# Kernel optimization log

Hardware: AMD Instinct MI355X
Metric: run time of the kernel (lower is better)

The kernel has to match this reference:

```python
import jax, jax.numpy as jnp
import numpy as np

N_NODES = 100000
N_EDGES = 1600000
EMB = 128
HID = 128
N_CLASSES = 10
N_GRAPHS = 512
EPS = 1e-5


def sage_conv(x, src, dst, Wl, Wr, b):
    # PyG SAGEConv: out = lin_l(mean_{j in N(i)} x_j) + lin_r(x_i)
    msg = x[src]  # [E, d] gather
    agg = jax.ops.segment_sum(msg, dst, num_segments=N_NODES)
    deg = jax.ops.segment_sum(jnp.ones((src.shape[0],), x.dtype), dst, num_segments=N_NODES)
    agg = agg / jnp.maximum(deg, 1.0)[:, None]
    return agg @ Wl + x @ Wr + b


def setup_inputs() -> dict:
    key = jax.random.key(0)
    ks = jax.random.split(key, 20)
    x = jax.random.normal(ks[0], (N_NODES, EMB), dtype=jnp.float32)
    edge_index = jax.random.randint(ks[1], (2, N_EDGES), 0, N_NODES, dtype=jnp.int64)
    batch = jnp.sort(jax.random.randint(ks[2], (N_NODES,), 0, N_GRAPHS, dtype=jnp.int64))
    s = lambda k, shp, fan: jax.random.normal(k, shp, dtype=jnp.float32) * (1.0 / np.sqrt(fan))
    inp = {
        'x': x, 'edge_index': edge_index, 'batch': batch,
        'bn_gamma': jnp.ones((EMB,), jnp.float32),
        'bn_beta': jnp.zeros((EMB,), jnp.float32),
        'bn_mean': jax.random.normal(ks[3], (EMB,), jnp.float32) * 0.1,
        'bn_var': jax.random.uniform(ks[4], (EMB,), jnp.float32, 0.5, 1.5),
        'Wl1': s(ks[5], (EMB, HID), EMB), 'Wr1': s(ks[6], (EMB, HID), EMB), 'b1': jnp.zeros((HID,), jnp.float32),
        'Wl2': s(ks[7], (HID, HID), HID), 'Wr2': s(ks[8], (HID, HID), HID), 'b2': jnp.zeros((HID,), jnp.float32),
        'Wl3': s(ks[9], (HID, HID), HID), 'Wr3': s(ks[10], (HID, HID), HID), 'b3': jnp.zeros((HID,), jnp.float32),
        'Wm1': s(ks[11], (HID, HID), HID), 'bm1': jnp.zeros((HID,), jnp.float32),
        'Wm2': s(ks[12], (HID, N_CLASSES), HID), 'bm2': jnp.zeros((N_CLASSES,), jnp.float32),
    }
    return inp


def reference(x, edge_index, batch, bn_gamma, bn_beta, bn_mean, bn_var,
              Wl1, Wr1, b1, Wl2, Wr2, b2, Wl3, Wr3, b3, Wm1, bm1, Wm2, bm2):
    src, dst = edge_index[0], edge_index[1]
    # BatchNorm (eval mode, running stats); dropout is identity in eval
    h = (x - bn_mean) * jax.lax.rsqrt(bn_var + EPS) * bn_gamma + bn_beta
    h = jax.nn.relu(sage_conv(h, src, dst, Wl1, Wr1, b1))
    h = jax.nn.relu(sage_conv(h, src, dst, Wl2, Wr2, b2))
    h = jax.nn.relu(sage_conv(h, src, dst, Wl3, Wr3, b3))
    # global mean pool over graphs
    summed = jax.ops.segment_sum(h, batch, num_segments=N_GRAPHS)
    counts = jax.ops.segment_sum(jnp.ones((h.shape[0],), h.dtype), batch, num_segments=N_GRAPHS)
    g = summed / jnp.maximum(counts, 1.0)[:, None]
    g = g @ Wm1 + bm1
    g = g @ Wm2 + bm2
    return jax.nn.log_softmax(g, axis=1)
```

## Files before the change

kernel.cpp:

```cpp
#include <hip/hip_runtime.h>

#define NN 100000
#define NE 1600000
#define CH 128
#define NG 512
#define NC 10
#define NBK 782
#define NBA 800
#define EPB 2000
#define WB  384
#define BB  12500
#define GB  391
#define BPB 64

typedef float floatx4 __attribute__((ext_vector_type(4)));
typedef float floatx2 __attribute__((ext_vector_type(2)));
union f8frag { uint2 u; long long l; };

__device__ __forceinline__ float b2f(unsigned short u) {
    return __uint_as_float(((unsigned)u) << 16);
}
__device__ __forceinline__ unsigned short f2b(float f) {
    unsigned u = __float_as_uint(f);
    u += 0x7FFFu + ((u >> 16) & 1u);
    return (unsigned short)(u >> 16);
}
__device__ __forceinline__ float wlo(unsigned w) { return __uint_as_float(w << 16); }
__device__ __forceinline__ float whi(unsigned w) { return __uint_as_float(w & 0xFFFF0000u); }

__device__ __forceinline__ float ldf(const void* p, long i, int isb) {
    return isb ? b2f(((const unsigned short*)p)[i]) : ((const float*)p)[i];
}
__device__ __forceinline__ int ldi(const void* p, long i, int is64) {
    const int* q = (const int*)p;
    return is64 ? q[2 * i] : q[i];
}
__device__ __forceinline__ unsigned pk4_fp8(float f0, float f1, float f2, float f3) {
    int u = 0;
    u = __builtin_amdgcn_cvt_pk_fp8_f32(f0, f1, u, false);
    u = __builtin_amdgcn_cvt_pk_fp8_f32(f2, f3, u, true);
    return (unsigned)u;
}
__device__ __forceinline__ unsigned char f2f8(float v) {
    return (unsigned char)(__builtin_amdgcn_cvt_pk_fp8_f32(v, v, 0, false) & 0xFF);
}
__device__ __forceinline__ int detect_isb(const void* gamma) {
    return (*(const unsigned*)gamma == 0x3F800000u) ? 0 : 1;
}
__device__ __forceinline__ int detect_is64(const void* eidx) {
    const unsigned* e = (const unsigned*)eidx;
    return ((e[1] | e[3] | e[5] | e[7]) == 0u) ? 1 : 0;
}

__global__ __launch_bounds__(256) void prep_k(const void* __restrict__ x, const void* __restrict__ gamma,
                     const void* __restrict__ beta, const void* __restrict__ mean,
                     const void* __restrict__ var, const void* __restrict__ eidx,
                     const void* __restrict__ batch,
                     const void* W1, const void* W2, const void* W3,
                     const void* W4, const void* W5, const void* W6,
                     unsigned char* __restrict__ WT8,
                     unsigned* __restrict__ f80,
                     int* __restrict__ gcnt,
                     int* __restrict__ gse) {
    __shared__ int hist[NBK];
    int isb = detect_isb(gamma);
    if (blockIdx.x < WB) {
        int idx = blockIdx.x * 256 + threadIdx.x;
        int w = idx >> 14;
        int k = (idx >> 7) & 127;
        int n = idx & 127;
        const void* W = (w == 0) ? W1 : (w == 1) ? W2 : (w == 2) ? W3
                      : (w == 3) ? W4 : (w == 4) ? W5 : W6;
        float v = ldf(W, (long)k * CH + n, isb);
        WT8[(w << 14) + n * CH + k] = f2f8(v);
        return;
    }
    if (blockIdx.x >= WB + BB + NBA) {
        int i = (blockIdx.x - (WB + BB + NBA)) * 256 + threadIdx.x;
        if (i >= NN) return;
        int is64 = detect_is64(eidx);
        int b1v = ldi(batch, i, is64);
        int b0v = (i == 0) ? -1 : ldi(batch, (long)i - 1, is64);
        for (int g = b0v + 1; g <= b1v; ++g) gse[g] = i;
        if (i == NN - 1)
            for (int g = b1v + 1; g <= NG; ++g) gse[g] = NN;
        return;
    }
    if (blockIdx.x >= WB + BB) {
        int pb = blockIdx.x - (WB + BB);
        int is64 = detect_is64(eidx);
        int t = threadIdx.x;
        for (int b = t; b < NBK; b += 256) hist[b] = 0;
        __syncthreads();
        long e0 = (long)pb * EPB;
        for (int i = t; i < EPB; i += 256) {
            int d = ldi(eidx, (long)NE + e0 + i, is64);
            atomicAdd(&hist[d >> 7], 1);
        }
        __syncthreads();
        for (int b = t; b < NBK; b += 256) gcnt[(long)pb * NBK + b] = hist[b];
        return;
    }
    long i4 = ((long)(blockIdx.x - WB) * 256 + threadIdx.x) * 4;
    if (i4 >= (long)NN * CH) return;
    int c = (int)(i4 & (CH - 1));
    float xv[4], g[4], b[4], m[4], v[4];
    if (isb) {
        uint2 U = *(const uint2*)((const unsigned short*)x + i4);
        xv[0] = wlo(U.x); xv[1] = whi(U.x); xv[2] = wlo(U.y); xv[3] = whi(U.y);
        uint2 G = *(const uint2*)((const unsigned short*)gamma + c);
        g[0] = wlo(G.x); g[1] = whi(G.x); g[2] = wlo(G.y); g[3] = whi(G.y);
        uint2 B = *(const uint2*)((const unsigned short*)beta + c);
        b[0] = wlo(B.x); b[1] = whi(B.x); b[2] = wlo(B.y); b[3] = whi(B.y);
        uint2 M = *(const uint2*)((const unsigned short*)mean + c);
        m[0] = wlo(M.x); m[1] = whi(M.x); m[2] = wlo(M.y); m[3] = whi(M.y);
        uint2 V = *(const uint2*)((const unsigned short*)var + c);
        v[0] = wlo(V.x); v[1] = whi(V.x); v[2] = wlo(V.y); v[3] = whi(V.y);
    } else {
        float4 X = *(const float4*)((const float*)x + i4);
        xv[0] = X.x; xv[1] = X.y; xv[2] = X.z; xv[3] = X.w;
        float4 G = *(const float4*)((const float*)gamma + c);
        g[0] = G.x; g[1] = G.y; g[2] = G.z; g[3] = G.w;
        float4 B = *(const float4*)((const float*)beta + c);
        b[0] = B.x; b[1] = B.y; b[2] = B.z; b[3] = B.w;
        float4 M = *(const float4*)((const float*)mean + c);
        m[0] = M.x; m[1] = M.y; m[2] = M.z; m[3] = M.w;
        float4 V = *(const float4*)((const float*)var + c);
        v[0] = V.x; v[1] = V.y; v[2] = V.z; v[3] = V.w;
    }
    float o[4];
#pragma unroll
    for (int j = 0; j < 4; ++j)
        o[j] = (xv[j] - m[j]) * rsqrtf(v[j] + 1e-5f) * g[j] + b[j];
    f80[i4 >> 2] = pk4_fp8(o[0], o[1], o[2], o[3]);
}

__global__ __launch_bounds__(64) void colscan_k(const int* __restrict__ gcnt,
                                                int* __restrict__ colscan,
                                                int* __restrict__ btot) {
    int b = blockIdx.x;
    int lane = threadIdx.x;
    int carry = 0;
    for (int base = 0; base < NBA; base += 64) {
        int blk = base + lane;
        int v = (blk < NBA) ? gcnt[(long)blk * NBK + b] : 0;
        int x = v;
        for (int off = 1; off < 64; off <<= 1) {
            int y = __shfl_up(x, off);
            if (lane >= off) x += y;
        }
        if (blk < NBA) colscan[(long)b * NBA + blk] = carry + x - v;
        carry += __shfl(x, 63);
    }
    if (lane == 0) btot[b] = carry;
}

__global__ __launch_bounds__(1024) void bscan_k(const int* __restrict__ btot,
                                                int* __restrict__ bbase) {
    __shared__ int s[1024];
    int t = threadIdx.x;
    int v = (t < NBK) ? btot[t] : 0;
    s[t] = v;
    __syncthreads();
    for (int off = 1; off < 1024; off <<= 1) {
        int add = (t >= off) ? s[t - off] : 0;
        __syncthreads();
        s[t] += add;
        __syncthreads();
    }
    if (t < NBK) bbase[t] = s[t] - v;
}

__global__ __launch_bounds__(256) void partC_k(const void* __restrict__ eidx,
                                               const int* __restrict__ colscan,
                                               const int* __restrict__ bbase,
                                               unsigned* __restrict__ epair) {
    __shared__ int pos[NBK];
    int is64 = detect_is64(eidx);
    int t = threadIdx.x;
    int pb = (int)(blockIdx.x & 7) * (NBA / 8) + (int)(blockIdx.x >> 3);
    for (int b = t; b < NBK; b += 256)
        pos[b] = bbase[b] + colscan[(long)b * NBA + pb];
    __syncthreads();
    long e0 = (long)pb * EPB;
    for (int i = t; i < EPB; i += 256) {
        int sv = ldi(eidx, e0 + i, is64);
        int d  = ldi(eidx, (long)NE + e0 + i, is64);
        int b = d >> 7;
        int p = atomicAdd(&pos[b], 1);
        epair[p] = ((unsigned)(d & 127) << 20) | (unsigned)sv;
    }
}

__global__ __launch_bounds__(256) void csrfill_k(const unsigned* __restrict__ epair,
                                                 const int* __restrict__ bbase,
                                                 const int* __restrict__ btot,
                                                 int* __restrict__ row_ptr,
                                                 int* __restrict__ esrc) {
    __shared__ int hist[128];
    __shared__ int s[128];
    __shared__ int wcur[128];
    int bkt = blockIdx.x;
    int t = threadIdx.x;
    if (t < 128) hist[t] = 0;
    __syncthreads();
    int e0 = bbase[bkt], n = btot[bkt];
    for (int i = t; i < n; i += 256) atomicAdd(&hist[epair[e0 + i] >> 20], 1);
    __syncthreads();
    int v = (t < 128) ? hist[t] : 0;
    if (t < 128) s[t] = v;
    for (int off = 1; off < 128; off <<= 1) {
        __syncthreads();
        int add = (t < 128 && t >= off) ? s[t - off] : 0;
        __syncthreads();
        if (t < 128) s[t] += add;
    }
    __syncthreads();
    if (t < 128) {
        int excl = s[t] - v;
        int node = (bkt << 7) + t;
        int base = e0 + excl;
        wcur[t] = base;
        if (node < NN) row_ptr[node] = base;
        if (node == 0) row_ptr[NN] = NE;
    }
    __syncthreads();
    for (int i = t; i < n; i += 256) {
        unsigned pv = epair[e0 + i];
        int q = atomicAdd(&wcur[pv >> 20], 1);
        esrc[q] = (int)(pv & 0xFFFFFu);
    }
}

__device__ __forceinline__ uint4 gld1(const uint4* __restrict__ f8in4,
                                      const int* __restrict__ esrc,
                                      int ee, int s1v, int h) {
    bool val = ee < s1v;
    int ec = max(min(ee, s1v - 1), 0);
    int idx = esrc[ec];
    idx = val ? idx : 0;
    uint4 u = f8in4[(size_t)idx * 8 + h];
    if (!val) { u.x = 0u; u.y = 0u; u.z = 0u; u.w = 0u; }
    return u;
}

#define ACC8(u) do { \
    a0 += __builtin_amdgcn_cvt_pk_f32_fp8((int)(u).x, false); \
    a1 += __builtin_amdgcn_cvt_pk_f32_fp8((int)(u).x, true);  \
    a2 += __builtin_amdgcn_cvt_pk_f32_fp8((int)(u).y, false); \
    a3 += __builtin_amdgcn_cvt_pk_f32_fp8((int)(u).y, true);  \
    a4 += __builtin_amdgcn_cvt_pk_f32_fp8((int)(u).z, false); \
    a5 += __builtin_amdgcn_cvt_pk_f32_fp8((int)(u).z, true);  \
    a6 += __builtin_amdgcn_cvt_pk_f32_fp8((int)(u).w, false); \
    a7 += __builtin_amdgcn_cvt_pk_f32_fp8((int)(u).w, true);  \
} while (0)

__global__ __launch_bounds__(1024, 8) void flayer_k(const uint4* __restrict__ f8in4,
                                                const int* __restrict__ row_ptr,
                                                const int* __restrict__ esrc,
                                                const uint4* __restrict__ Wl4,
                                                const uint4* __restrict__ Wr4,
                                                const void* __restrict__ bias,
                                                const void* __restrict__ gamma,
                                                unsigned char* __restrict__ out8) {
    __shared__ unsigned char WlS[16384];
    __shared__ unsigned char WrS[16384];
    __shared__ unsigned char Ag[BPB][144];
    __shared__ unsigned char Sf[BPB][144];
    const int tid = threadIdx.x;
    const int wv = tid >> 6;
    const int lane = tid & 63;
    const int sub = lane >> 4;
    const int l15 = lane & 15;
    const int row0 = blockIdx.x * BPB;

    {
        int wrow = tid >> 3, h16 = (tid & 7) * 16;
        int dst = wrow * 128 + (h16 ^ ((wrow & 7) << 4));
        *(uint4*)&WlS[dst] = Wl4[tid];
        *(uint4*)&WrS[dst] = Wr4[tid];
    }
    if (tid < BPB * 8) {
        int r = tid >> 3, h = tid & 7;
        int rs = min(row0 + r, NN - 1);
        *(uint4*)&Sf[r][h * 16] = f8in4[(size_t)rs * 8 + h];
    }

    const int nl = wv * 4 + sub;
    const int node = row0 + nl;
    const int nc = min(node, NN - 1);
    const int s0 = row_ptr[nc];
    const int s1v = (node < NN) ? row_ptr[nc + 1] : s0;
    const int par = l15 >> 3;
    const int h = l15 & 7;
    floatx2 a0 = {0.f, 0.f}, a1 = {0.f, 0.f}, a2 = {0.f, 0.f}, a3 = {0.f, 0.f};
    floatx2 a4 = {0.f, 0.f}, a5 = {0.f, 0.f}, a6 = {0.f, 0.f}, a7 = {0.f, 0.f};
    uint4 q0, q1, q2, q3;
    int ee = s0 + par;
    q0 = gld1(f8in4, esrc, ee,     s1v, h);
    q1 = gld1(f8in4, esrc, ee + 2, s1v, h);
    q2 = gld1(f8in4, esrc, ee + 4, s1v, h);
    q3 = gld1(f8in4, esrc, ee + 6, s1v, h);
    ee += 8;
    for (;;) {
        if (!__any(ee < s1v)) break;
        ACC8(q0); q0 = gld1(f8in4, esrc, ee, s1v, h); ee += 2;
        if (!__any(ee < s1v)) break;
        ACC8(q1); q1 = gld1(f8in4, esrc, ee, s1v, h); ee += 2;
        if (!__any(ee < s1v)) break;
        ACC8(q2); q2 = gld1(f8in4, esrc, ee, s1v, h); ee += 2;
        if (!__any(ee < s1v)) break;
        ACC8(q3); q3 = gld1(f8in4, esrc, ee, s1v, h); ee += 2;
    }
    ACC8(q0); ACC8(q1); ACC8(q2); ACC8(q3);
#define CMB(x) do { x[0] += __shfl_xor(x[0], 8); x[1] += __shfl_xor(x[1], 8); } while (0)
    CMB(a0); CMB(a1); CMB(a2); CMB(a3); CMB(a4); CMB(a5); CMB(a6); CMB(a7);
#undef CMB
    if (par == 0) {
        float inv = 1.0f / (float)max(s1v - s0, 1);
        uint4 o;
        o.x = pk4_fp8(a0[0] * inv, a0[1] * inv, a1[0] * inv, a1[1] * inv);
        o.y = pk4_fp8(a2[0] * inv, a2[1] * inv, a3[0] * inv, a3[1] * inv);
        o.z = pk4_fp8(a4[0] * inv, a4[1] * inv, a5[0] * inv, a5[1] * inv);
        o.w = pk4_fp8(a6[0] * inv, a6[1] * inv, a7[0] * inv, a7[1] * inv);
        *(uint4*)&Ag[nl][h * 16] = o;
    }
    __syncthreads();

    const int rt0 = (wv >> 2) * 16;
    const int n0 = (wv & 3) * 32;
    const int quad = sub;
    floatx4 acc[2];
    acc[0] = (floatx4)0.f; acc[1] = (floatx4)0.f;
#pragma unroll
    for (int chunk = 0; chunk < 8; ++chunk) {
        const unsigned char* WS = (chunk < 4) ? WlS : WrS;
        const int k8 = ((chunk & 3) * 4 + quad) * 8;
        const int r0 = n0 + l15;
        const int r1 = n0 + 16 + l15;
        f8frag b0, b1, a;
        b0.u = *(const uint2*)&WS[r0 * 128 + (k8 ^ ((r0 & 7) << 4))];
        b1.u = *(const uint2*)&WS[r1 * 128 + (k8 ^ ((r1 & 7) << 4))];
        if (chunk < 4) a.u = *(const uint2*)&Ag[rt0 + l15][k8];
        else           a.u = *(const uint2*)&Sf[rt0 + l15][k8];
        acc[0] = __builtin_amdgcn_mfma_f32_16x16x32_fp8_fp8(a.l, b0.l, acc[0], 0, 0, 0);
        acc[1] = __builtin_amdgcn_mfma_f32_16x16x32_fp8_fp8(a.l, b1.l, acc[1], 0, 0, 0);
    }
    const int isb = detect_isb(gamma);
    float bv0 = ldf(bias, n0 + l15, isb);
    float bv1 = ldf(bias, n0 + 16 + l15, isb);
    __syncthreads();
#pragma unroll
    for (int tc = 0; tc < 2; ++tc) {
        int col = n0 + tc * 16 + l15;
        float bv = tc ? bv1 : bv0;
#pragma unroll
        for (int r = 0; r < 4; ++r) {
            int row = rt0 + quad * 4 + r;
            Ag[row][col] = f2f8(fmaxf(acc[tc][r] + bv, 0.f));
        }
    }
    __syncthreads();
    if (tid < BPB * 8) {
        int r = tid >> 3, h2 = tid & 7;
        if (row0 + r < NN)
            *(uint4*)(out8 + (size_t)(row0 + r) * CH + h2 * 16) = *(const uint4*)&Ag[r][h2 * 16];
    }
}

__global__ __launch_bounds__(512) void poolmlp_k(const uint2* __restrict__ f8h,
                                                 const int* __restrict__ gse,
                                                 const void* __restrict__ gamma,
                                                 const void* __restrict__ Wm1, const void* __restrict__ bm1,
                                                 const void* __restrict__ Wm2, const void* __restrict__ bm2,
                                                 void* __restrict__ dout) {
    int g = blockIdx.x;
    int t = threadIdx.x;
    int wv = t >> 6;
    int lane = t & 63;
    int sub = lane >> 4;
    int l15 = lane & 15;
    int isb = detect_isb(gamma);
    __shared__ float red[8][128];
    __shared__ float pl[CH];
    __shared__ float hv[CH];
    __shared__ float logit[NC];
    __shared__ float lse;
    int s0 = gse[g], s1 = gse[g + 1];
    floatx2 a0 = {0.f, 0.f}, a1 = {0.f, 0.f}, a2 = {0.f, 0.f}, a3 = {0.f, 0.f};
    for (int n = s0 + wv * 4 + sub; n < s1; n += 32) {
        uint2 u = f8h[n * 16 + l15];
        a0 += __builtin_amdgcn_cvt_pk_f32_fp8((int)u.x, false);
        a1 += __builtin_amdgcn_cvt_pk_f32_fp8((int)u.x, true);
        a2 += __builtin_amdgcn_cvt_pk_f32_fp8((int)u.y, false);
        a3 += __builtin_amdgcn_cvt_pk_f32_fp8((int)u.y, true);
    }
#pragma unroll
    for (int sh = 16; sh <= 32; sh <<= 1) {
        a0[0] += __shfl_xor(a0[0], sh); a0[1] += __shfl_xor(a0[1], sh);
        a1[0] += __shfl_xor(a1[0], sh); a1[1] += __shfl_xor(a1[1], sh);
        a2[0] += __shfl_xor(a2[0], sh); a2[1] += __shfl_xor(a2[1], sh);
        a3[0] += __shfl_xor(a3[0], sh); a3[1] += __shfl_xor(a3[1], sh);
    }
    if (sub == 0) {
        int c = l15 * 8;
        red[wv][c + 0] = a0[0]; red[wv][c + 1] = a0[1];
        red[wv][c + 2] = a1[0]; red[wv][c + 3] = a1[1];
        red[wv][c + 4] = a2[0]; red[wv][c + 5] = a2[1];
        red[wv][c + 6] = a3[0]; red[wv][c + 7] = a3[1];
    }
    __syncthreads();
    if (t < CH) {
        float s = 0.f;
#pragma unroll
        for (int w = 0; w < 8; ++w) s += red[w][t];
        pl[t] = s / (float)max(s1 - s0, 1);
    }
    __syncthreads();
    if (t < CH) {
        float acc = ldf(bm1, t, isb);
        for (int k = 0; k < CH; ++k) acc += pl[k] * ldf(Wm1, (long)k * CH + t, isb);
        hv[t] = acc;
    }
    __syncthreads();
    if (t < NC) {
        float a2v = ldf(bm2, t, isb);
        for (int k = 0; k < CH; ++k) a2v += hv[k] * ldf(Wm2, (long)k * NC + t, isb);
        logit[t] = a2v;
    }
    __syncthreads();
    if (t == 0) {
        float m = -1e30f;
        for (int i = 0; i < NC; ++i) m = fmaxf(m, logit[i]);
        float s = 0.f;
        for (int i = 0; i < NC; ++i) s += expf(logit[i] - m);
        lse = m + logf(s);
    }
    __syncthreads();
    if (t < NC) {
        float o = logit[t] - lse;
        if (isb) ((unsigned short*)dout)[g * NC + t] = f2b(o);
        else     ((float*)dout)[g * NC + t] = o;
    }
}

extern "C" void kernel_launch(void* const* d_in, const int* in_sizes, int n_in,
                              void* d_out, int out_size, void* d_ws, size_t ws_size,
                              hipStream_t stream) {
    const void* x     = d_in[0];
    const void* eidx  = d_in[1];
    const void* batch = d_in[2];
    const void* gamma = d_in[3];
    const void* beta  = d_in[4];
    const void* mean  = d_in[5];
    const void* var   = d_in[6];
    const void* Wl1 = d_in[7],  *Wr1 = d_in[8],  *b1 = d_in[9];
    const void* Wl2 = d_in[10], *Wr2 = d_in[11], *b2 = d_in[12];
    const void* Wl3 = d_in[13], *Wr3 = d_in[14], *b3 = d_in[15];
    const void* Wm1 = d_in[16], *bm1 = d_in[17], *Wm2 = d_in[18], *bm2 = d_in[19];

    char* ws = (char*)d_ws;
    size_t off = 0;
    auto alloc = [&](size_t bytes) -> void* {
        void* p = (void*)(ws + off);
        off = (off + bytes + 255) & ~(size_t)255;
        return p;
    };
    int*   row_ptr = (int*)alloc((size_t)(NN + 1) * 4);
    int*   esrc    = (int*)alloc((size_t)NE * 4);
    unsigned* epair = (unsigned*)alloc((size_t)NE * 4);
    int*   btot    = (int*)alloc((size_t)NBK * 4);
    int*   bbase   = (int*)alloc((size_t)NBK * 4);
    int*   gse     = (int*)alloc((size_t)(NG + 1) * 4);
    unsigned char* WT8 = (unsigned char*)alloc((size_t)6 * CH * CH);
    unsigned char* f8A = (unsigned char*)alloc((size_t)NN * CH);
    unsigned char* f8B = (unsigned char*)alloc((size_t)NN * CH);
    (void)ws_size; (void)in_sizes; (void)n_in; (void)out_size;

    int* gcnt    = (int*)f8B;
    int* colscan = (int*)(f8B + (((size_t)NBA * NBK * 4 + 255) & ~(size_t)255));

    prep_k<<<WB + BB + NBA + GB, 256, 0, stream>>>(x, gamma, beta, mean, var, eidx, batch,
                                                   Wl1, Wr1, Wl2, Wr2, Wl3, Wr3,
                                                   WT8, (unsigned*)f8A, gcnt, gse);
    colscan_k<<<NBK, 64, 0, stream>>>(gcnt, colscan, btot);
    bscan_k<<<1, 1024, 0, stream>>>(btot, bbase);
    partC_k<<<NBA, 256, 0, stream>>>(eidx, colscan, bbase, epair);
    csrfill_k<<<NBK, 256, 0, stream>>>(epair, bbase, btot, row_ptr, esrc);

    const uint4* W4l1 = (const uint4*)(WT8 + 0 * CH * CH);
    const uint4* W4r1 = (const uint4*)(WT8 + 1 * CH * CH);
    const uint4* W4l2 = (const uint4*)(WT8 + 2 * CH * CH);
    const uint4* W4r2 = (const uint4*)(WT8 + 3 * CH * CH);
    const uint4* W4l3 = (const uint4*)(WT8 + 4 * CH * CH);
    const uint4* W4r3 = (const uint4*)(WT8 + 5 * CH * CH);

    const int fl_grid = (NN + BPB - 1) / BPB;

    flayer_k<<<fl_grid, 1024, 0, stream>>>((const uint4*)f8A, row_ptr, esrc,
                                           W4l1, W4r1, b1, gamma, f8B);
    flayer_k<<<fl_grid, 1024, 0, stream>>>((const uint4*)f8B, row_ptr, esrc,
                                           W4l2, W4r2, b2, gamma, f8A);
    flayer_k<<<fl_grid, 1024, 0, stream>>>((const uint4*)f8A, row_ptr, esrc,
                                           W4l3, W4r3, b3, gamma, f8B);

    poolmlp_k<<<NG, 512, 0, stream>>>((const uint2*)f8B, gse, gamma,
                                      Wm1, bm1, Wm2, bm2, d_out);
}
```

Before: 359.2 us.

## Split fused SAGE layer into plane-major gather and GEMM kernels

Stores fp8 node features in four 32-channel planes instead of row-major 128-byte rows. Each fused layer kernel becomes a gather kernel, which averages one plane per block over neighbors, and a separate GEMM kernel that reads the aggregated buffer. Gathering one plane at a time shrinks the working set of random neighbor reads so it may stay in cache. The cost is an extra kernel launch per layer and a write plus re-read of the aggregate buffer, which reuses the edge-pair scratch memory.

```diff
diff --git a/kernel.cpp b/kernel.cpp
--- a/kernel.cpp
+++ b/kernel.cpp
@@ -12,6 +12,7 @@
 #define BB  12500
 #define GB  391
 #define BPB 64
+#define PLN ((size_t)NN * 4)
 
 typedef float floatx4 __attribute__((ext_vector_type(4)));
 typedef float floatx2 __attribute__((ext_vector_type(2)));
@@ -132,7 +133,9 @@
 #pragma unroll
     for (int j = 0; j < 4; ++j)
         o[j] = (xv[j] - m[j]) * rsqrtf(v[j] + 1e-5f) * g[j] + b[j];
-    f80[i4 >> 2] = pk4_fp8(o[0], o[1], o[2], o[3]);
+    int nodei = (int)(i4 >> 7);
+    f80[(size_t)(c >> 5) * NN * 8 + (size_t)nodei * 8 + ((c & 31) >> 2)] =
+        pk4_fp8(o[0], o[1], o[2], o[3]);
 }
 
 __global__ __launch_bounds__(64) void colscan_k(const int* __restrict__ gcnt,
@@ -232,14 +235,14 @@
     }
 }
 
-__device__ __forceinline__ uint4 gld1(const uint4* __restrict__ f8in4,
+__device__ __forceinline__ uint4 gld1(const uint4* __restrict__ pb,
                                       const int* __restrict__ esrc,
-                                      int ee, int s1v, int h) {
+                                      int ee, int s1v) {
     bool val = ee < s1v;
     int ec = max(min(ee, s1v - 1), 0);
     int idx = esrc[ec];
     idx = val ? idx : 0;
-    uint4 u = f8in4[(size_t)idx * 8 + h];
+    uint4 u = pb[(size_t)idx * 2];
     if (!val) { u.x = 0u; u.y = 0u; u.z = 0u; u.w = 0u; }
     return u;
 }
@@ -255,14 +258,64 @@
     a7 += __builtin_amdgcn_cvt_pk_f32_fp8((int)(u).w, true);  \
 } while (0)
 
-__global__ __launch_bounds__(1024, 8) void flayer_k(const uint4* __restrict__ f8in4,
-                                                const int* __restrict__ row_ptr,
-                                                const int* __restrict__ esrc,
-                                                const uint4* __restrict__ Wl4,
-                                                const uint4* __restrict__ Wr4,
-                                                const void* __restrict__ bias,
-                                                const void* __restrict__ gamma,
-                                                unsigned char* __restrict__ out8) {
+__global__ __launch_bounds__(256, 8) void gather_k(const uint4* __restrict__ f8p,
+                                                   const int* __restrict__ row_ptr,
+                                                   const int* __restrict__ esrc,
+                                                   uint4* __restrict__ agg8) {
+    const int tid = threadIdx.x;
+    const int wv = tid >> 6;
+    const int lane = tid & 63;
+    const int sub = lane >> 4;
+    const int l15 = lane & 15;
+    const int h = l15 & 1;
+    const int e = l15 >> 1;
+    const unsigned bid = blockIdx.x;
+    const int plane = (int)((bid >> 1) & 3);
+    const int row0 = (int)((bid >> 3) * 32 + (bid & 1) * 16);
+    const int node = row0 + wv * 4 + sub;
+    const int s0 = row_ptr[node];
+    const int s1v = row_ptr[node + 1];
+    const uint4* __restrict__ pb = f8p + (size_t)plane * (NN * 2) + h;
+
+    floatx2 a0 = {0.f, 0.f}, a1 = {0.f, 0.f}, a2 = {0.f, 0.f}, a3 = {0.f, 0.f};
+    floatx2 a4 = {0.f, 0.f}, a5 = {0.f, 0.f}, a6 = {0.f, 0.f}, a7 = {0.f, 0.f};
+    int ee = s0 + e;
+    uint4 q0 = gld1(pb, esrc, ee, s1v);
+    uint4 q1 = gld1(pb, esrc, ee + 8, s1v);
+    ee += 16;
+    for (;;) {
+        if (!__any(ee < s1v)) break;
+        ACC8(q0); q0 = gld1(pb, esrc, ee, s1v); ee += 8;
+        if (!__any(ee < s1v)) break;
+        ACC8(q1); q1 = gld1(pb, esrc, ee, s1v); ee += 8;
+    }
+    ACC8(q0); ACC8(q1);
+
+#define CMB(x, sh) do { x[0] += __shfl_xor(x[0], sh); x[1] += __shfl_xor(x[1], sh); } while (0)
+#pragma unroll
+    for (int sh = 2; sh <= 8; sh <<= 1) {
+        CMB(a0, sh); CMB(a1, sh); CMB(a2, sh); CMB(a3, sh);
+        CMB(a4, sh); CMB(a5, sh); CMB(a6, sh); CMB(a7, sh);
+    }
+#undef CMB
+    if (e == 0) {
+        float inv = 1.0f / (float)max(s1v - s0, 1);
+        uint4 o;
+        o.x = pk4_fp8(a0[0] * inv, a0[1] * inv, a1[0] * inv, a1[1] * inv);
+        o.y = pk4_fp8(a2[0] * inv, a2[1] * inv, a3[0] * inv, a3[1] * inv);
+        o.z = pk4_fp8(a4[0] * inv, a4[1] * inv, a5[0] * inv, a5[1] * inv);
+        o.w = pk4_fp8(a6[0] * inv, a6[1] * inv, a7[0] * inv, a7[1] * inv);
+        agg8[(size_t)plane * (NN * 2) + (size_t)node * 2 + h] = o;
+    }
+}
+
+__global__ __launch_bounds__(1024, 8) void gemm_k(const uint4* __restrict__ f8self,
+                                                  const uint4* __restrict__ agg8,
+                                                  const uint4* __restrict__ Wl4,
+                                                  const uint4* __restrict__ Wr4,
+                                                  const void* __restrict__ bias,
+                                                  const void* __restrict__ gamma,
+                                                  unsigned char* __restrict__ out8) {
     __shared__ unsigned char WlS[16384];
     __shared__ unsigned char WrS[16384];
     __shared__ unsigned char Ag[BPB][144];
@@ -280,50 +333,14 @@
         *(uint4*)&WlS[dst] = Wl4[tid];
         *(uint4*)&WrS[dst] = Wr4[tid];
     }
-    if (tid < BPB * 8) {
-        int r = tid >> 3, h = tid & 7;
+    {
+        int t2 = tid & 511;
+        int r = t2 >> 3, hh = t2 & 7;
+        int p = hh >> 1, half = hh & 1;
         int rs = min(row0 + r, NN - 1);
-        *(uint4*)&Sf[r][h * 16] = f8in4[(size_t)rs * 8 + h];
-    }
-
-    const int nl = wv * 4 + sub;
-    const int node = row0 + nl;
-    const int nc = min(node, NN - 1);
-    const int s0 = row_ptr[nc];
-    const int s1v = (node < NN) ? row_ptr[nc + 1] : s0;
-    const int par = l15 >> 3;
-    const int h = l15 & 7;
-    floatx2 a0 = {0.f, 0.f}, a1 = {0.f, 0.f}, a2 = {0.f, 0.f}, a3 = {0.f, 0.f};
-    floatx2 a4 = {0.f, 0.f}, a5 = {0.f, 0.f}, a6 = {0.f, 0.f}, a7 = {0.f, 0.f};
-    uint4 q0, q1, q2, q3;
-    int ee = s0 + par;
-    q0 = gld1(f8in4, esrc, ee,     s1v, h);
-    q1 = gld1(f8in4, esrc, ee + 2, s1v, h);
-    q2 = gld1(f8in4, esrc, ee + 4, s1v, h);
-    q3 = gld1(f8in4, esrc, ee + 6, s1v, h);
-    ee += 8;
-    for (;;) {
-        if (!__any(ee < s1v)) break;
-        ACC8(q0); q0 = gld1(f8in4, esrc, ee, s1v, h); ee += 2;
-        if (!__any(ee < s1v)) break;
-        ACC8(q1); q1 = gld1(f8in4, esrc, ee, s1v, h); ee += 2;
-        if (!__any(ee < s1v)) break;
-        ACC8(q2); q2 = gld1(f8in4, esrc, ee, s1v, h); ee += 2;
-        if (!__any(ee < s1v)) break;
-        ACC8(q3); q3 = gld1(f8in4, esrc, ee, s1v, h); ee += 2;
-    }
-    ACC8(q0); ACC8(q1); ACC8(q2); ACC8(q3);
-#define CMB(x) do { x[0] += __shfl_xor(x[0], 8); x[1] += __shfl_xor(x[1], 8); } while (0)
-    CMB(a0); CMB(a1); CMB(a2); CMB(a3); CMB(a4); CMB(a5); CMB(a6); CMB(a7);
-#undef CMB
-    if (par == 0) {
-        float inv = 1.0f / (float)max(s1v - s0, 1);
-        uint4 o;
-        o.x = pk4_fp8(a0[0] * inv, a0[1] * inv, a1[0] * inv, a1[1] * inv);
-        o.y = pk4_fp8(a2[0] * inv, a2[1] * inv, a3[0] * inv, a3[1] * inv);
-        o.z = pk4_fp8(a4[0] * inv, a4[1] * inv, a5[0] * inv, a5[1] * inv);
-        o.w = pk4_fp8(a6[0] * inv, a6[1] * inv, a7[0] * inv, a7[1] * inv);
-        *(uint4*)&Ag[nl][h * 16] = o;
+        size_t pidx = (size_t)p * (NN * 2) + (size_t)rs * 2 + half;
+        if (tid < 512) *(uint4*)&Sf[r][hh * 16] = f8self[pidx];
+        else           *(uint4*)&Ag[r][hh * 16] = agg8[pidx];
     }
     __syncthreads();
 
@@ -364,7 +381,8 @@
     if (tid < BPB * 8) {
         int r = tid >> 3, h2 = tid & 7;
         if (row0 + r < NN)
-            *(uint4*)(out8 + (size_t)(row0 + r) * CH + h2 * 16) = *(const uint4*)&Ag[r][h2 * 16];
+            *(uint4*)(out8 + (size_t)(h2 >> 1) * NN * 32 + (size_t)(row0 + r) * 32 + (h2 & 1) * 16)
+                = *(const uint4*)&Ag[r][h2 * 16];
     }
 }
 
@@ -388,8 +406,9 @@
     __shared__ float lse;
     int s0 = gse[g], s1 = gse[g + 1];
     floatx2 a0 = {0.f, 0.f}, a1 = {0.f, 0.f}, a2 = {0.f, 0.f}, a3 = {0.f, 0.f};
+    size_t pbase = (size_t)(l15 >> 2) * PLN + (l15 & 3);
     for (int n = s0 + wv * 4 + sub; n < s1; n += 32) {
-        uint2 u = f8h[n * 16 + l15];
+        uint2 u = f8h[pbase + (size_t)n * 4];
         a0 += __builtin_amdgcn_cvt_pk_f32_fp8((int)u.x, false);
         a1 += __builtin_amdgcn_cvt_pk_f32_fp8((int)u.x, true);
         a2 += __builtin_amdgcn_cvt_pk_f32_fp8((int)u.y, false);
@@ -468,7 +487,7 @@
     };
     int*   row_ptr = (int*)alloc((size_t)(NN + 1) * 4);
     int*   esrc    = (int*)alloc((size_t)NE * 4);
-    unsigned* epair = (unsigned*)alloc((size_t)NE * 4);
+    unsigned char* unionbuf = (unsigned char*)alloc((size_t)NN * CH);
     int*   btot    = (int*)alloc((size_t)NBK * 4);
     int*   bbase   = (int*)alloc((size_t)NBK * 4);
     int*   gse     = (int*)alloc((size_t)(NG + 1) * 4);
@@ -477,6 +496,10 @@
     unsigned char* f8B = (unsigned char*)alloc((size_t)NN * CH);
     (void)ws_size; (void)in_sizes; (void)n_in; (void)out_size;
 
+    unsigned* epair = (unsigned*)unionbuf;
+    const uint4* agg8 = (const uint4*)unionbuf;
+    uint4* agg8w = (uint4*)unionbuf;
+
     int* gcnt    = (int*)f8B;
     int* colscan = (int*)(f8B + (((size_t)NBA * NBK * 4 + 255) & ~(size_t)255));
 
@@ -495,14 +518,17 @@
     const uint4* W4l3 = (const uint4*)(WT8 + 4 * CH * CH);
     const uint4* W4r3 = (const uint4*)(WT8 + 5 * CH * CH);
 
-    const int fl_grid = (NN + BPB - 1) / BPB;
-
-    flayer_k<<<fl_grid, 1024, 0, stream>>>((const uint4*)f8A, row_ptr, esrc,
-                                           W4l1, W4r1, b1, gamma, f8B);
-    flayer_k<<<fl_grid, 1024, 0, stream>>>((const uint4*)f8B, row_ptr, esrc,
-                                           W4l2, W4r2, b2, gamma, f8A);
-    flayer_k<<<fl_grid, 1024, 0, stream>>>((const uint4*)f8A, row_ptr, esrc,
-                                           W4l3, W4r3, b3, gamma, f8B);
+    const int ga_grid = (NN / 16) * 4;
+    const int ge_grid = (NN + BPB - 1) / BPB;
+
+    gather_k<<<ga_grid, 256, 0, stream>>>((const uint4*)f8A, row_ptr, esrc, agg8w);
+    gemm_k<<<ge_grid, 1024, 0, stream>>>((const uint4*)f8A, agg8, W4l1, W4r1, b1, gamma, f8B);
+
+    gather_k<<<ga_grid, 256, 0, stream>>>((const uint4*)f8B, row_ptr, esrc, agg8w);
+    gemm_k<<<ge_grid, 1024, 0, stream>>>((const uint4*)f8B, agg8, W4l2, W4r2, b2, gamma, f8A);
+
+    gather_k<<<ga_grid, 256, 0, stream>>>((const uint4*)f8A, row_ptr, esrc, agg8w);
+    gemm_k<<<ge_grid, 1024, 0, stream>>>((const uint4*)f8A, agg8, W4l3, W4r3, b3, gamma, f8B);
 
     poolmlp_k<<<NG, 512, 0, stream>>>((const uint2*)f8B, gse, gamma,
                                       Wm1, bm1, Wm2, bm2, d_out);
```

New measurement: 424.4 us. 18.2% more time.

## Replace bucketed two-pass CSR build with global-atomic degree count and direct scatter

Applied to the files above, without the earlier changes.

The CSR construction moves from a two-level bucket scheme (per-block histograms, column scan, bucket partition, per-bucket fill) to a per-node degree count with global atomics, a three-kernel prefix scan, and a direct atomic scatter of source indices. BatchNorm coefficients are also precomputed once into a scale/shift table so the feature-prep pass does one FMA per element. The aim is fewer passes over the edge list and less intermediate traffic. In exchange it relies on heavy global atomic contention on random destinations, and the order of neighbours within each row becomes nondeterministic.

```diff
diff --git a/kernel.cpp b/kernel.cpp
--- a/kernel.cpp
+++ b/kernel.cpp
@@ -5,13 +5,13 @@
 #define CH 128
 #define NG 512
 #define NC 10
-#define NBK 782
 #define NBA 800
 #define EPB 2000
 #define WB  384
 #define BB  12500
 #define GB  391
 #define BPB 64
+#define NSB 98
 
 typedef float floatx4 __attribute__((ext_vector_type(4)));
 typedef float floatx2 __attribute__((ext_vector_type(2)));
@@ -52,17 +52,39 @@
     return ((e[1] | e[3] | e[5] | e[7]) == 0u) ? 1 : 0;
 }
 
-__global__ __launch_bounds__(256) void prep_k(const void* __restrict__ x, const void* __restrict__ gamma,
-                     const void* __restrict__ beta, const void* __restrict__ mean,
-                     const void* __restrict__ var, const void* __restrict__ eidx,
+__global__ __launch_bounds__(256) void coef_k(const void* __restrict__ gamma,
+                                              const void* __restrict__ beta,
+                                              const void* __restrict__ mean,
+                                              const void* __restrict__ var,
+                                              float* __restrict__ ab,
+                                              int* __restrict__ deg) {
+    if (blockIdx.x == 0) {
+        int t = threadIdx.x;
+        if (t < CH) {
+            int isb = detect_isb(gamma);
+            float g = ldf(gamma, t, isb), b = ldf(beta, t, isb);
+            float m = ldf(mean, t, isb), v = ldf(var, t, isb);
+            float a = g * rsqrtf(v + 1e-5f);
+            ab[t] = a;
+            ab[CH + t] = b - m * a;
+        }
+        return;
+    }
+    int i = (int)(blockIdx.x - 1) * 256 + threadIdx.x;
+    if (i < NN) deg[i] = 0;
+}
+
+__global__ __launch_bounds__(256) void prep_k(const void* __restrict__ x,
+                     const float* __restrict__ ab,
+                     const void* __restrict__ eidx,
                      const void* __restrict__ batch,
+                     const void* __restrict__ gamma,
                      const void* W1, const void* W2, const void* W3,
                      const void* W4, const void* W5, const void* W6,
                      unsigned char* __restrict__ WT8,
                      unsigned* __restrict__ f80,
-                     int* __restrict__ gcnt,
+                     int* __restrict__ deg,
                      int* __restrict__ gse) {
-    __shared__ int hist[NBK];
     int isb = detect_isb(gamma);
     if (blockIdx.x < WB) {
         int idx = blockIdx.x * 256 + threadIdx.x;
@@ -89,77 +111,37 @@
     if (blockIdx.x >= WB + BB) {
         int pb = blockIdx.x - (WB + BB);
         int is64 = detect_is64(eidx);
-        int t = threadIdx.x;
-        for (int b = t; b < NBK; b += 256) hist[b] = 0;
-        __syncthreads();
         long e0 = (long)pb * EPB;
-        for (int i = t; i < EPB; i += 256) {
+        for (int i = threadIdx.x; i < EPB; i += 256) {
             int d = ldi(eidx, (long)NE + e0 + i, is64);
-            atomicAdd(&hist[d >> 7], 1);
+            atomicAdd(&deg[d], 1);
         }
-        __syncthreads();
-        for (int b = t; b < NBK; b += 256) gcnt[(long)pb * NBK + b] = hist[b];
         return;
     }
     long i4 = ((long)(blockIdx.x - WB) * 256 + threadIdx.x) * 4;
     if (i4 >= (long)NN * CH) return;
     int c = (int)(i4 & (CH - 1));
-    float xv[4], g[4], b[4], m[4], v[4];
+    float4 A = *(const float4*)(ab + c);
+    float4 Bv = *(const float4*)(ab + CH + c);
+    float xv[4];
     if (isb) {
         uint2 U = *(const uint2*)((const unsigned short*)x + i4);
         xv[0] = wlo(U.x); xv[1] = whi(U.x); xv[2] = wlo(U.y); xv[3] = whi(U.y);
-        uint2 G = *(const uint2*)((const unsigned short*)gamma + c);
-        g[0] = wlo(G.x); g[1] = whi(G.x); g[2] = wlo(G.y); g[3] = whi(G.y);
-        uint2 B = *(const uint2*)((const unsigned short*)beta + c);
-        b[0] = wlo(B.x); b[1] = whi(B.x); b[2] = wlo(B.y); b[3] = whi(B.y);
-        uint2 M = *(const uint2*)((const unsigned short*)mean + c);
-        m[0] = wlo(M.x); m[1] = whi(M.x); m[2] = wlo(M.y); m[3] = whi(M.y);
-        uint2 V = *(const uint2*)((const unsigned short*)var + c);
-        v[0] = wlo(V.x); v[1] = whi(V.x); v[2] = wlo(V.y); v[3] = whi(V.y);
     } else {
         float4 X = *(const float4*)((const float*)x + i4);
         xv[0] = X.x; xv[1] = X.y; xv[2] = X.z; xv[3] = X.w;
-        float4 G = *(const float4*)((const float*)gamma + c);
-        g[0] = G.x; g[1] = G.y; g[2] = G.z; g[3] = G.w;
-        float4 B = *(const float4*)((const float*)beta + c);
-        b[0] = B.x; b[1] = B.y; b[2] = B.z; b[3] = B.w;
-        float4 M = *(const float4*)((const float*)mean + c);
-        m[0] = M.x; m[1] = M.y; m[2] = M.z; m[3] = M.w;
-        float4 V = *(const float4*)((const float*)var + c);
-        v[0] = V.x; v[1] = V.y; v[2] = V.z; v[3] = V.w;
-    }
-    float o[4];
-#pragma unroll
-    for (int j = 0; j < 4; ++j)
-        o[j] = (xv[j] - m[j]) * rsqrtf(v[j] + 1e-5f) * g[j] + b[j];
-    f80[i4 >> 2] = pk4_fp8(o[0], o[1], o[2], o[3]);
-}
-
-__global__ __launch_bounds__(64) void colscan_k(const int* __restrict__ gcnt,
-                                                int* __restrict__ colscan,
-                                                int* __restrict__ btot) {
-    int b = blockIdx.x;
-    int lane = threadIdx.x;
-    int carry = 0;
-    for (int base = 0; base < NBA; base += 64) {
-        int blk = base + lane;
-        int v = (blk < NBA) ? gcnt[(long)blk * NBK + b] : 0;
-        int x = v;
-        for (int off = 1; off < 64; off <<= 1) {
-            int y = __shfl_up(x, off);
-            if (lane >= off) x += y;
-        }
-        if (blk < NBA) colscan[(long)b * NBA + blk] = carry + x - v;
-        carry += __shfl(x, 63);
-    }
-    if (lane == 0) btot[b] = carry;
-}
-
-__global__ __launch_bounds__(1024) void bscan_k(const int* __restrict__ btot,
-                                                int* __restrict__ bbase) {
+    }
+    f80[i4 >> 2] = pk4_fp8(xv[0] * A.x + Bv.x, xv[1] * A.y + Bv.y,
+                           xv[2] * A.z + Bv.z, xv[3] * A.w + Bv.w);
+}
+
+__global__ __launch_bounds__(1024) void scan1_k(const int* __restrict__ deg,
+                                                int* __restrict__ row_ptr,
+                                                int* __restrict__ bsum) {
     __shared__ int s[1024];
-    int t = threadIdx.x;
-    int v = (t < NBK) ? btot[t] : 0;
+    int b = blockIdx.x, t = threadIdx.x;
+    int i = b * 1024 + t;
+    int v = (i < NN) ? deg[i] : 0;
     s[t] = v;
     __syncthreads();
     for (int off = 1; off < 1024; off <<= 1) {
@@ -168,67 +150,49 @@
         s[t] += add;
         __syncthreads();
     }
-    if (t < NBK) bbase[t] = s[t] - v;
-}
-
-__global__ __launch_bounds__(256) void partC_k(const void* __restrict__ eidx,
-                                               const int* __restrict__ colscan,
-                                               const int* __restrict__ bbase,
-                                               unsigned* __restrict__ epair) {
-    __shared__ int pos[NBK];
+    if (i < NN) row_ptr[i] = s[t] - v;
+    if (t == 1023) bsum[b] = s[t];
+}
+
+__global__ __launch_bounds__(128) void scan2_k(const int* __restrict__ bsum,
+                                               int* __restrict__ gbase) {
+    __shared__ int s[128];
+    int t = threadIdx.x;
+    int v = (t < NSB) ? bsum[t] : 0;
+    s[t] = v;
+    __syncthreads();
+    for (int off = 1; off < 128; off <<= 1) {
+        int add = (t >= off) ? s[t - off] : 0;
+        __syncthreads();
+        s[t] += add;
+        __syncthreads();
+    }
+    if (t < NSB) gbase[t] = s[t] - v;
+}
+
+__global__ __launch_bounds__(1024) void fix_k(int* __restrict__ row_ptr,
+                                              const int* __restrict__ gbase,
+                                              int* __restrict__ pos) {
+    int b = blockIdx.x, t = threadIdx.x;
+    int i = b * 1024 + t;
+    if (i < NN) {
+        int r = row_ptr[i] + gbase[b];
+        row_ptr[i] = r;
+        pos[i] = r;
+    }
+    if (i == 0) row_ptr[NN] = NE;
+}
+
+__global__ __launch_bounds__(256) void scatter_k(const void* __restrict__ eidx,
+                                                 int* __restrict__ pos,
+                                                 int* __restrict__ esrc) {
     int is64 = detect_is64(eidx);
-    int t = threadIdx.x;
-    int pb = (int)(blockIdx.x & 7) * (NBA / 8) + (int)(blockIdx.x >> 3);
-    for (int b = t; b < NBK; b += 256)
-        pos[b] = bbase[b] + colscan[(long)b * NBA + pb];
-    __syncthreads();
-    long e0 = (long)pb * EPB;
-    for (int i = t; i < EPB; i += 256) {
+    long e0 = (long)blockIdx.x * EPB;
+    for (int i = threadIdx.x; i < EPB; i += 256) {
         int sv = ldi(eidx, e0 + i, is64);
         int d  = ldi(eidx, (long)NE + e0 + i, is64);
-        int b = d >> 7;
-        int p = atomicAdd(&pos[b], 1);
-        epair[p] = ((unsigned)(d & 127) << 20) | (unsigned)sv;
-    }
-}
-
-__global__ __launch_bounds__(256) void csrfill_k(const unsigned* __restrict__ epair,
-                                                 const int* __restrict__ bbase,
-                                                 const int* __restrict__ btot,
-                                                 int* __restrict__ row_ptr,
-                                                 int* __restrict__ esrc) {
-    __shared__ int hist[128];
-    __shared__ int s[128];
-    __shared__ int wcur[128];
-    int bkt = blockIdx.x;
-    int t = threadIdx.x;
-    if (t < 128) hist[t] = 0;
-    __syncthreads();
-    int e0 = bbase[bkt], n = btot[bkt];
-    for (int i = t; i < n; i += 256) atomicAdd(&hist[epair[e0 + i] >> 20], 1);
-    __syncthreads();
-    int v = (t < 128) ? hist[t] : 0;
-    if (t < 128) s[t] = v;
-    for (int off = 1; off < 128; off <<= 1) {
-        __syncthreads();
-        int add = (t < 128 && t >= off) ? s[t - off] : 0;
-        __syncthreads();
-        if (t < 128) s[t] += add;
-    }
-    __syncthreads();
-    if (t < 128) {
-        int excl = s[t] - v;
-        int node = (bkt << 7) + t;
-        int base = e0 + excl;
-        wcur[t] = base;
-        if (node < NN) row_ptr[node] = base;
-        if (node == 0) row_ptr[NN] = NE;
-    }
-    __syncthreads();
-    for (int i = t; i < n; i += 256) {
-        unsigned pv = epair[e0 + i];
-        int q = atomicAdd(&wcur[pv >> 20], 1);
-        esrc[q] = (int)(pv & 0xFFFFFu);
+        int p = atomicAdd(&pos[d], 1);
+        esrc[p] = sv;
     }
 }
 
@@ -468,25 +432,25 @@
     };
     int*   row_ptr = (int*)alloc((size_t)(NN + 1) * 4);
     int*   esrc    = (int*)alloc((size_t)NE * 4);
-    unsigned* epair = (unsigned*)alloc((size_t)NE * 4);
-    int*   btot    = (int*)alloc((size_t)NBK * 4);
-    int*   bbase   = (int*)alloc((size_t)NBK * 4);
+    int*   deg     = (int*)alloc((size_t)NN * 4);
+    int*   pos     = (int*)alloc((size_t)NN * 4);
+    int*   bsum    = (int*)alloc((size_t)256 * 4);
+    int*   gbase   = (int*)alloc((size_t)256 * 4);
     int*   gse     = (int*)alloc((size_t)(NG + 1) * 4);
+    float* ab      = (float*)alloc((size_t)2 * CH * 4);
     unsigned char* WT8 = (unsigned char*)alloc((size_t)6 * CH * CH);
     unsigned char* f8A = (unsigned char*)alloc((size_t)NN * CH);
     unsigned char* f8B = (unsigned char*)alloc((size_t)NN * CH);
     (void)ws_size; (void)in_sizes; (void)n_in; (void)out_size;
 
-    int* gcnt    = (int*)f8B;
-    int* colscan = (int*)(f8B + (((size_t)NBA * NBK * 4 + 255) & ~(size_t)255));
-
-    prep_k<<<WB + BB + NBA + GB, 256, 0, stream>>>(x, gamma, beta, mean, var, eidx, batch,
+    coef_k<<<1 + (NN + 255) / 256, 256, 0, stream>>>(gamma, beta, mean, var, ab, deg);
+    prep_k<<<WB + BB + NBA + GB, 256, 0, stream>>>(x, ab, eidx, batch, gamma,
                                                    Wl1, Wr1, Wl2, Wr2, Wl3, Wr3,
-                                                   WT8, (unsigned*)f8A, gcnt, gse);
-    colscan_k<<<NBK, 64, 0, stream>>>(gcnt, colscan, btot);
-    bscan_k<<<1, 1024, 0, stream>>>(btot, bbase);
-    partC_k<<<NBA, 256, 0, stream>>>(eidx, colscan, bbase, epair);
-    csrfill_k<<<NBK, 256, 0, stream>>>(epair, bbase, btot, row_ptr, esrc);
+                                                   WT8, (unsigned*)f8A, deg, gse);
+    scan1_k<<<NSB, 1024, 0, stream>>>(deg, row_ptr, bsum);
+    scan2_k<<<1, 128, 0, stream>>>(bsum, gbase);
+    fix_k<<<NSB, 1024, 0, stream>>>(row_ptr, gbase, pos);
+    scatter_k<<<NBA, 256, 0, stream>>>(eidx, pos, esrc);
 
     const uint4* W4l1 = (const uint4*)(WT8 + 0 * CH * CH);
     const uint4* W4r1 = (const uint4*)(WT8 + 1 * CH * CH);
```

Measured after the change: 522.5 us. +45.4%, slower.
